# Optimization experiments

Hardware: AMD Instinct MI355X
Metric: run time of the kernel (lower is better)

## Reference

```python
import jax, jax.numpy as jnp
import numpy as np

D_MODEL = 1024
N_HEADS = 16
D_K = D_MODEL // N_HEADS
B, S = 2, 2048


def setup_inputs() -> dict:
    key = jax.random.key(0)
    ks = jax.random.split(key, 5)
    x = jax.random.normal(ks[0], (B, S, D_MODEL), dtype=jnp.float32)
    # causal 0/1 mask, broadcastable over batch and heads
    mask = jnp.tril(jnp.ones((S, S), dtype=jnp.int32))[None, None, :, :]
    scale = 1.0 / np.sqrt(D_MODEL)
    w_qkv_w = jax.random.normal(ks[1], (3 * D_MODEL, D_MODEL), dtype=jnp.float32) * scale
    w_qkv_b = jnp.zeros((3 * D_MODEL,), dtype=jnp.float32)
    w_o_w = jax.random.normal(ks[2], (D_MODEL, D_MODEL), dtype=jnp.float32) * scale
    w_o_b = jnp.zeros((D_MODEL,), dtype=jnp.float32)
    return {"x": x, "mask": mask, "w_qkv_w": w_qkv_w, "w_qkv_b": w_qkv_b,
            "w_o_w": w_o_w, "w_o_b": w_o_b}


def reference(x, mask, w_qkv_w, w_qkv_b, w_o_w, w_o_b):
    b, s, d = x.shape
    qkv = x @ w_qkv_w.T + w_qkv_b                       # [b, s, 3d]
    q, k, v = jnp.split(qkv, 3, axis=-1)
    # [b, h, s, dk]
    q = q.reshape(b, s, N_HEADS, D_K).transpose(0, 2, 1, 3)
    k = k.reshape(b, s, N_HEADS, D_K).transpose(0, 2, 1, 3)
    v = v.reshape(b, s, N_HEADS, D_K).transpose(0, 2, 1, 3)
    scores = jnp.einsum('bhqd,bhkd->bhqk', q, k) / jnp.sqrt(jnp.float32(D_K))
    scores = jnp.where(mask == 0, jnp.float32(-1e9), scores)
    attn = jax.nn.softmax(scores, axis=-1)
    out = jnp.einsum('bhqk,bhkd->bhqd', attn, v)        # [b, h, s, dk]
    out = out.transpose(0, 2, 1, 3).reshape(b, s, d)
    return out @ w_o_w.T + w_o_b
```

## Files before the change

kernel.cpp:

```cpp
#include <hip/hip_runtime.h>
#include <cstdint>
#include <cstddef>


typedef __attribute__((ext_vector_type(8))) short bf16x8;
typedef __attribute__((ext_vector_type(4))) float f32x4;
typedef __attribute__((ext_vector_type(4))) unsigned int u32x4;
typedef __attribute__((ext_vector_type(4))) unsigned short u16x4;
typedef __attribute__((ext_vector_type(8))) unsigned short u16x8;

__device__ __forceinline__ unsigned short f2b(float f) {
  unsigned int u = __float_as_uint(f);
  u = u + 0x7FFFu + ((u >> 16) & 1u);
  return (unsigned short)(u >> 16);
}
__device__ __forceinline__ unsigned short f2b_trunc(float f) {
  return (unsigned short)(__float_as_uint(f) >> 16);
}

__device__ __forceinline__ void gl_lds16(const unsigned short* g, unsigned short* s) {
  __builtin_amdgcn_global_load_lds((const __attribute__((address_space(1))) void*)g,
                                   (__attribute__((address_space(3))) void*)s, 16, 0, 0);
}

__global__ __launch_bounds__(256) void cvt_all(const float* __restrict__ x,
                                               const float* __restrict__ wq,
                                               const float* __restrict__ wo,
                                               unsigned short* __restrict__ xb,
                                               unsigned short* __restrict__ wqb,
                                               unsigned short* __restrict__ wob) {
  const int bid = blockIdx.x;
  const float* in;
  unsigned short* out;
  int base;
  if (bid < 4096)      { in = x;  out = xb;  base = bid; }
  else if (bid < 7168) { in = wq; out = wqb; base = bid - 4096; }
  else                 { in = wo; out = wob; base = bid - 7168; }
  const int idx = (base * 256 + threadIdx.x) * 4;
  f32x4 v = *(const f32x4*)(in + idx);
  u16x4 r;
  r[0] = f2b(v[0]); r[1] = f2b(v[1]); r[2] = f2b(v[2]); r[3] = f2b(v[3]);
  *(u16x4*)(out + idx) = r;
}

__global__ __launch_bounds__(256) void gemm_bt(const unsigned short* __restrict__ A,
                                               const unsigned short* __restrict__ W,
                                               const float* __restrict__ bias,
                                               unsigned short* __restrict__ Cb,
                                               unsigned short* __restrict__ vtb,
                                               int M, int N, int K, int qcols) {
  __shared__ unsigned short As[2][128 * 32];
  __shared__ unsigned short Bs[2][128 * 32];
  const int tid  = threadIdx.x;
  const int lane = tid & 63;
  const int w    = tid >> 6;
  const int wy   = w >> 1, wx = w & 1;
  const int l15  = lane & 15, quad = lane >> 4;
  const int xr2  = (l15 >> 1) & 3;
  const int m0 = blockIdx.y * 128, n0 = blockIdx.x * 128;

  const unsigned short* gA[2];
  const unsigned short* gB[2];
  int off[2];
#pragma unroll
  for (int p = 0; p < 2; ++p) {
    const int c = tid + p * 256;
    const int r = c >> 2;
    const int srcc = (c & 3) ^ ((r >> 1) & 3);
    gA[p] = A + (size_t)(m0 + r) * K + srcc * 8;
    gB[p] = W + (size_t)(n0 + r) * K + srcc * 8;
    off[p] = c * 8;
  }

  f32x4 acc[4][4];
#pragma unroll
  for (int i = 0; i < 4; ++i)
#pragma unroll
    for (int j = 0; j < 4; ++j) acc[i][j] = (f32x4){0.f, 0.f, 0.f, 0.f};

#pragma unroll
  for (int p = 0; p < 2; ++p) {
    gl_lds16(gA[p], &As[0][off[p]]);
    gl_lds16(gB[p], &Bs[0][off[p]]);
  }

  const int NIT = K >> 5;
  for (int it = 0; it < NIT; ++it) {
    __syncthreads();
    const int cur = it & 1;
    if (it + 1 < NIT) {
      const int kt = (it + 1) << 5;
#pragma unroll
      for (int p = 0; p < 2; ++p) {
        gl_lds16(gA[p] + kt, &As[cur ^ 1][off[p]]);
        gl_lds16(gB[p] + kt, &Bs[cur ^ 1][off[p]]);
      }
    }
    const unsigned short* Ac = As[cur];
    const unsigned short* Bc = Bs[cur];
    bf16x8 af[4], bfr[4];
#pragma unroll
    for (int i = 0; i < 4; ++i)
      af[i] = *(const bf16x8*)&Ac[(wy * 64 + i * 16 + l15) * 32 + (quad ^ xr2) * 8];
#pragma unroll
    for (int j = 0; j < 4; ++j)
      bfr[j] = *(const bf16x8*)&Bc[(wx * 64 + j * 16 + l15) * 32 + (quad ^ xr2) * 8];
#pragma unroll
    for (int i = 0; i < 4; ++i)
#pragma unroll
      for (int j = 0; j < 4; ++j)
        acc[i][j] = __builtin_amdgcn_mfma_f32_16x16x32_bf16(af[i], bfr[j], acc[i][j], 0, 0, 0);
  }

  const bool vblock = (n0 >= 2048);
#pragma unroll
  for (int i = 0; i < 4; ++i) {
    const int row = m0 + wy * 64 + i * 16 + quad * 4;
#pragma unroll
    for (int j = 0; j < 4; ++j) {
      const int col = n0 + wx * 64 + j * 16 + l15;
      const float bv = bias[col];
      if (!vblock) {
        const float sc = (col < qcols) ? 0.125f : 1.0f;
#pragma unroll
        for (int r = 0; r < 4; ++r)
          Cb[(size_t)(row + r) * N + col] = f2b((acc[i][j][r] + bv) * sc);
      } else {
        const int hd = col - 2048;
        const int bb = row >> 11, s = row & 2047;
        u16x4 ov;
#pragma unroll
        for (int r = 0; r < 4; ++r) ov[r] = f2b(acc[i][j][r] + bv);
        *(u16x4*)(vtb + ((size_t)(bb * 1024 + hd)) * 2048 + s) = ov;
      }
    }
  }
}

__global__ __launch_bounds__(256) void gemm_bt64(const unsigned short* __restrict__ A,
                                                 const unsigned short* __restrict__ W,
                                                 const float* __restrict__ bias,
                                                 float* __restrict__ Cf,
                                                 int M, int N, int K) {
  __shared__ unsigned short As[2][128 * 64];
  __shared__ unsigned short Bs[2][64 * 64];
  const int tid  = threadIdx.x;
  const int lane = tid & 63;
  const int w    = tid >> 6;
  const int wy   = w >> 1, wx = w & 1;
  const int l15  = lane & 15, quad = lane >> 4;
  const int xr   = l15 & 7;
  const int m0 = blockIdx.y * 128, n0 = blockIdx.x * 64;

  const unsigned short* gA[4];
  int offA[4];
#pragma unroll
  for (int p = 0; p < 4; ++p) {
    const int c = tid + p * 256;
    const int r = c >> 3;
    const int sc = ((c & 7) ^ (r & 7)) * 8;
    gA[p] = A + (size_t)(m0 + r) * K + sc;
    offA[p] = c * 8;
  }
  const unsigned short* gB[2];
  int offB[2];
#pragma unroll
  for (int p = 0; p < 2; ++p) {
    const int c = tid + p * 256;
    const int r = c >> 3;
    const int sc = ((c & 7) ^ (r & 7)) * 8;
    gB[p] = W + (size_t)(n0 + r) * K + sc;
    offB[p] = c * 8;
  }

  f32x4 acc[4][2];
#pragma unroll
  for (int i = 0; i < 4; ++i)
#pragma unroll
    for (int j = 0; j < 2; ++j) acc[i][j] = (f32x4){0.f, 0.f, 0.f, 0.f};

#pragma unroll
  for (int p = 0; p < 4; ++p) gl_lds16(gA[p], &As[0][offA[p]]);
#pragma unroll
  for (int p = 0; p < 2; ++p) gl_lds16(gB[p], &Bs[0][offB[p]]);

  const int NIT = K >> 6;
  for (int it = 0; it < NIT; ++it) {
    __syncthreads();
    const int cur = it & 1;
    if (it + 1 < NIT) {
      const int kt = (it + 1) << 6;
#pragma unroll
      for (int p = 0; p < 4; ++p) gl_lds16(gA[p] + kt, &As[cur ^ 1][offA[p]]);
#pragma unroll
      for (int p = 0; p < 2; ++p) gl_lds16(gB[p] + kt, &Bs[cur ^ 1][offB[p]]);
    }
    const unsigned short* Ac = As[cur];
    const unsigned short* Bc = Bs[cur];
#pragma unroll
    for (int kc = 0; kc < 2; ++kc) {
      bf16x8 af[4], bfr[2];
#pragma unroll
      for (int i = 0; i < 4; ++i)
        af[i] = *(const bf16x8*)&Ac[(wy * 64 + i * 16 + l15) * 64 + ((kc * 4 + quad) ^ xr) * 8];
#pragma unroll
      for (int j = 0; j < 2; ++j)
        bfr[j] = *(const bf16x8*)&Bc[(wx * 32 + j * 16 + l15) * 64 + ((kc * 4 + quad) ^ xr) * 8];
#pragma unroll
      for (int i = 0; i < 4; ++i)
#pragma unroll
        for (int j = 0; j < 2; ++j)
          acc[i][j] = __builtin_amdgcn_mfma_f32_16x16x32_bf16(af[i], bfr[j], acc[i][j], 0, 0, 0);
    }
  }

#pragma unroll
  for (int i = 0; i < 4; ++i) {
    const int row = m0 + wy * 64 + i * 16 + quad * 4;
#pragma unroll
    for (int j = 0; j < 2; ++j) {
      const int col = n0 + wx * 32 + j * 16 + l15;
      const float bv = bias[col];
#pragma unroll
      for (int r = 0; r < 4; ++r)
        Cf[(size_t)(row + r) * N + col] = acc[i][j][r] + bv;
    }
  }
}

__global__ __launch_bounds__(256, 3) void attn_fwd(const unsigned short* __restrict__ qkv,
                                                   const unsigned short* __restrict__ vt,
                                                   unsigned short* __restrict__ o) {
  __shared__ unsigned short Ks[2][64 * 64];
  __shared__ unsigned short Vs[2][64 * 64];
  __shared__ unsigned short pbuf[4][2][16 * 40];
  const int tid  = threadIdx.x;
  const int lane = tid & 63;
  const int w    = tid >> 6;
  const int wq   = w & 1;
  const int wk   = w >> 1;
  const int l15  = lane & 15, quad = lane >> 4;
  const int xr   = l15 & 7;
  const int bh = blockIdx.x, b = bh >> 4, h = bh & 15;
  const int y  = (int)blockIdx.y;
  const int qt = (y < 16) ? y : 47 - y;
  const int q0 = qt * 64;
  const int T = qt + 1;
  const int qs0 = q0 + wq * 32;
  const int qs1 = qs0 + 16;

  const unsigned short* gKd[2];
  const unsigned short* gVd[2];
  int doff[2];
#pragma unroll
  for (int p = 0; p < 2; ++p) {
    const int c = tid + p * 256;
    const int r = c >> 3;
    const int sc = ((c & 7) ^ (r & 7)) * 8;
    gKd[p] = qkv + (size_t)(b * 2048 + r) * 3072 + 1024 + h * 64 + sc;
    gVd[p] = vt + (size_t)(bh * 64 + r) * 2048 + sc;
    doff[p] = c * 8;
  }

  const unsigned short* qr0 = qkv + (size_t)(b * 2048 + qs0 + l15) * 3072 + h * 64;
  const unsigned short* qr1 = qkv + (size_t)(b * 2048 + qs1 + l15) * 3072 + h * 64;
  const bf16x8 bq[2][2] = {
    { *(const bf16x8*)(qr0 + quad * 8), *(const bf16x8*)(qr0 + 32 + quad * 8) },
    { *(const bf16x8*)(qr1 + quad * 8), *(const bf16x8*)(qr1 + 32 + quad * 8) } };

  bf16x8 vones;
#pragma unroll
  for (int k = 0; k < 8; ++k) vones[k] = (short)0x3F80;

  f32x4 acc[2][4];
#pragma unroll
  for (int i = 0; i < 2; ++i)
#pragma unroll
    for (int j = 0; j < 4; ++j) acc[i][j] = (f32x4){0.f, 0.f, 0.f, 0.f};
  f32x4 accL[2] = {(f32x4){0.f, 0.f, 0.f, 0.f}, (f32x4){0.f, 0.f, 0.f, 0.f}};

  unsigned short* P0 = pbuf[w][0];
  unsigned short* P1 = pbuf[w][1];

#pragma unroll
  for (int p = 0; p < 2; ++p) {
    gl_lds16(gKd[p], &Ks[0][doff[p]]);
    gl_lds16(gVd[p], &Vs[0][doff[p]]);
  }

  for (int t = 0; t < T; ++t) {
    __syncthreads();
    const int cur = t & 1;
    if (t + 1 < T) {
      const size_t ko = (size_t)(t + 1) * 64 * 3072;
      const int vo = (t + 1) * 64;
#pragma unroll
      for (int p = 0; p < 2; ++p) {
        gl_lds16(gKd[p] + ko, &Ks[cur ^ 1][doff[p]]);
        gl_lds16(gVd[p] + vo, &Vs[cur ^ 1][doff[p]]);
      }
    }
    const unsigned short* Kc = Ks[cur];
    const unsigned short* Vc = Vs[cur];
    const int kv0 = t * 64 + wk * 32;

    bf16x8 kA[2][2];
#pragma unroll
    for (int n = 0; n < 2; ++n) {
      const int row = wk * 32 + n * 16 + l15;
      kA[n][0] = *(const bf16x8*)&Kc[row * 64 + ((quad) ^ xr) * 8];
      kA[n][1] = *(const bf16x8*)&Kc[row * 64 + ((4 + quad) ^ xr) * 8];
    }
    f32x4 st[2][2];
#pragma unroll
    for (int s = 0; s < 2; ++s)
#pragma unroll
      for (int n = 0; n < 2; ++n) {
        f32x4 z = (f32x4){0.f, 0.f, 0.f, 0.f};
        z = __builtin_amdgcn_mfma_f32_16x16x32_bf16(kA[n][0], bq[s][0], z, 0, 0, 0);
        z = __builtin_amdgcn_mfma_f32_16x16x32_bf16(kA[n][1], bq[s][1], z, 0, 0, 0);
        st[s][n] = z;
      }
    bf16x8 av[4];
#pragma unroll
    for (int j = 0; j < 4; ++j) {
      const int row = j * 16 + l15;
      av[j] = *(const bf16x8*)&Vc[row * 64 + ((wk * 4 + quad) ^ xr) * 8];
    }
#pragma unroll
    for (int s = 0; s < 2; ++s) {
      unsigned short* P = s ? P1 : P0;
      const int qbase = s ? qs1 : qs0;
      if (kv0 + 31 > qbase) {
        const int qrow = qbase + l15;
#pragma unroll
        for (int n = 0; n < 2; ++n)
#pragma unroll
          for (int r = 0; r < 4; ++r)
            if (kv0 + n * 16 + quad * 4 + r > qrow) st[s][n][r] = -1e30f;
      }
#pragma unroll
      for (int n = 0; n < 2; ++n) {
#pragma unroll
        for (int r = 0; r < 4; ++r) st[s][n][r] = __expf(st[s][n][r]);
        u16x4 pw;
        pw[0] = f2b_trunc(st[s][n][0]); pw[1] = f2b_trunc(st[s][n][1]);
        pw[2] = f2b_trunc(st[s][n][2]); pw[3] = f2b_trunc(st[s][n][3]);
        *(u16x4*)&P[l15 * 40 + n * 16 + quad * 4] = pw;
      }
    }
#pragma unroll
    for (int s = 0; s < 2; ++s) {
      const unsigned short* P = s ? P1 : P0;
      const bf16x8 bp = *(const bf16x8*)&P[l15 * 40 + quad * 8];
      accL[s] = __builtin_amdgcn_mfma_f32_16x16x32_bf16(vones, bp, accL[s], 0, 0, 0);
#pragma unroll
      for (int j = 0; j < 4; ++j)
        acc[s][j] = __builtin_amdgcn_mfma_f32_16x16x32_bf16(av[j], bp, acc[s][j], 0, 0, 0);
    }
  }

  __syncthreads();
  float* cmbA = (float*)&Ks[0][0];
  float* cmbL = (float*)&Vs[0][0];
  if (wk == 1) {
#pragma unroll
    for (int s = 0; s < 2; ++s) {
      cmbL[(wq * 2 + s) * 64 + lane] = accL[s][0];
#pragma unroll
      for (int j = 0; j < 4; ++j)
        *(f32x4*)&cmbA[(((wq * 2 + s) * 4 + j) << 8) + lane * 4] = acc[s][j];
    }
  }
  __syncthreads();
  if (wk == 0) {
#pragma unroll
    for (int s = 0; s < 2; ++s) {
      const float lsum = accL[s][0] + cmbL[(wq * 2 + s) * 64 + lane];
      const float inv = 1.0f / lsum;
      const int qrow = (s ? qs1 : qs0) + l15;
      unsigned short* orow = o + (size_t)(b * 2048 + qrow) * 1024 + h * 64;
#pragma unroll
      for (int j = 0; j < 4; ++j) {
        const f32x4 oth = *(const f32x4*)&cmbA[(((wq * 2 + s) * 4 + j) << 8) + lane * 4];
        u16x4 ov;
        ov[0] = f2b((acc[s][j][0] + oth[0]) * inv);
        ov[1] = f2b((acc[s][j][1] + oth[1]) * inv);
        ov[2] = f2b((acc[s][j][2] + oth[2]) * inv);
        ov[3] = f2b((acc[s][j][3] + oth[3]) * inv);
        *(u16x4*)(orow + j * 16 + quad * 4) = ov;
      }
    }
  }
}

extern "C" void kernel_launch(void* const* d_in, const int* in_sizes, int n_in,
                              void* d_out, int out_size, void* d_ws, size_t ws_size,
                              hipStream_t stream) {
  const float* x       = (const float*)d_in[0];
  const float* w_qkv_w = (const float*)d_in[2];
  const float* w_qkv_b = (const float*)d_in[3];
  const float* w_o_w   = (const float*)d_in[4];
  const float* w_o_b   = (const float*)d_in[5];
  float* out = (float*)d_out;

  unsigned short* ws    = (unsigned short*)d_ws;
  unsigned short* xb    = ws;
  unsigned short* wqb   = xb   + (size_t)4096 * 1024;
  unsigned short* wob   = wqb  + (size_t)3072 * 1024;
  unsigned short* qkvb  = wob  + (size_t)1024 * 1024;
  unsigned short* vtb   = qkvb + (size_t)4096 * 3072;
  unsigned short* attnb = vtb  + (size_t)2048 * 2048;

  cvt_all<<<8192, 256, 0, stream>>>(x, w_qkv_w, w_o_w, xb, wqb, wob);
  gemm_bt<<<dim3(24, 32), 256, 0, stream>>>(xb, wqb, w_qkv_b, qkvb, vtb, 4096, 3072, 1024, 1024);
  attn_fwd<<<dim3(32, 32), 256, 0, stream>>>(qkvb, vtb, attnb);
  gemm_bt64<<<dim3(16, 32), 256, 0, stream>>>(attnb, wob, w_o_b, out, 4096, 1024, 1024);
}
```

Measured before the change: 179.1 us.

## Replace QKV GEMM with 256x256 tile, 8-wave pipelined kernel

Rewrites the QKV projection GEMM to use 256x256 block tiles with 512 threads, a K-step of 64, and a hand-scheduled double buffer. Global-to-LDS loads are split into quarters and interleaved between MFMA groups, with explicit vmcnt waits, raw barriers and s_setprio. This aims to raise arithmetic intensity and overlap memory with compute. The cost is far fewer blocks (192) than CUs and large LDS use per block, which may leave compute units idle.

```diff
diff --git a/kernel.cpp b/kernel.cpp
--- a/kernel.cpp
+++ b/kernel.cpp
@@ -21,6 +21,12 @@
 __device__ __forceinline__ void gl_lds16(const unsigned short* g, unsigned short* s) {
   __builtin_amdgcn_global_load_lds((const __attribute__((address_space(1))) void*)g,
                                    (__attribute__((address_space(3))) void*)s, 16, 0, 0);
+}
+
+__device__ __forceinline__ void barrier_mem() {
+  asm volatile("" ::: "memory");
+  __builtin_amdgcn_s_barrier();
+  asm volatile("" ::: "memory");
 }
 
 __global__ __launch_bounds__(256) void cvt_all(const float* __restrict__ x,
@@ -43,94 +49,145 @@
   *(u16x4*)(out + idx) = r;
 }
 
-__global__ __launch_bounds__(256) void gemm_bt(const unsigned short* __restrict__ A,
-                                               const unsigned short* __restrict__ W,
-                                               const float* __restrict__ bias,
-                                               unsigned short* __restrict__ Cb,
-                                               unsigned short* __restrict__ vtb,
-                                               int M, int N, int K, int qcols) {
-  __shared__ unsigned short As[2][128 * 32];
-  __shared__ unsigned short Bs[2][128 * 32];
+__global__ __launch_bounds__(512, 2) void gemm8(const unsigned short* __restrict__ A,
+                                                const unsigned short* __restrict__ W,
+                                                const float* __restrict__ bias,
+                                                unsigned short* __restrict__ Cb,
+                                                unsigned short* __restrict__ vtb,
+                                                int M, int N, int K, int qcols) {
+  __shared__ unsigned short As[2][256 * 64];
+  __shared__ unsigned short Bs[2][256 * 64];
   const int tid  = threadIdx.x;
   const int lane = tid & 63;
   const int w    = tid >> 6;
-  const int wy   = w >> 1, wx = w & 1;
+  const int wm   = w >> 2;
+  const int wn   = w & 3;
   const int l15  = lane & 15, quad = lane >> 4;
-  const int xr2  = (l15 >> 1) & 3;
-  const int m0 = blockIdx.y * 128, n0 = blockIdx.x * 128;
-
-  const unsigned short* gA[2];
-  const unsigned short* gB[2];
-  int off[2];
-#pragma unroll
-  for (int p = 0; p < 2; ++p) {
-    const int c = tid + p * 256;
-    const int r = c >> 2;
-    const int srcc = (c & 3) ^ ((r >> 1) & 3);
-    gA[p] = A + (size_t)(m0 + r) * K + srcc * 8;
-    gB[p] = W + (size_t)(n0 + r) * K + srcc * 8;
-    off[p] = c * 8;
-  }
-
-  f32x4 acc[4][4];
-#pragma unroll
-  for (int i = 0; i < 4; ++i)
+  const int xr   = l15 & 7;
+  const int m0 = blockIdx.y * 256, n0 = blockIdx.x * 256;
+
+  const int r    = tid >> 3;
+  const int slot = (tid & 7) ^ (r & 7);
+  const unsigned short* gAq = A + (size_t)(m0 + r) * K + slot * 8;
+  const unsigned short* gBq = W + (size_t)(n0 + r) * K + slot * 8;
+  const int coff = tid * 8;
+
+  f32x4 acc[8][4];
+#pragma unroll
+  for (int i = 0; i < 8; ++i)
 #pragma unroll
     for (int j = 0; j < 4; ++j) acc[i][j] = (f32x4){0.f, 0.f, 0.f, 0.f};
 
-#pragma unroll
-  for (int p = 0; p < 2; ++p) {
-    gl_lds16(gA[p], &As[0][off[p]]);
-    gl_lds16(gB[p], &Bs[0][off[p]]);
-  }
-
-  const int NIT = K >> 5;
-  for (int it = 0; it < NIT; ++it) {
-    __syncthreads();
-    const int cur = it & 1;
-    if (it + 1 < NIT) {
-      const int kt = (it + 1) << 5;
-#pragma unroll
-      for (int p = 0; p < 2; ++p) {
-        gl_lds16(gA[p] + kt, &As[cur ^ 1][off[p]]);
-        gl_lds16(gB[p] + kt, &Bs[cur ^ 1][off[p]]);
-      }
-    }
-    const unsigned short* Ac = As[cur];
-    const unsigned short* Bc = Bs[cur];
-    bf16x8 af[4], bfr[4];
-#pragma unroll
-    for (int i = 0; i < 4; ++i)
-      af[i] = *(const bf16x8*)&Ac[(wy * 64 + i * 16 + l15) * 32 + (quad ^ xr2) * 8];
+  const size_t q64K = (size_t)64 * K;
+#pragma unroll
+  for (int qb = 0; qb < 4; ++qb)
+    gl_lds16(gBq + (size_t)qb * q64K, &Bs[0][qb * 4096 + coff]);
+  gl_lds16(gAq + 0 * q64K, &As[0][0 * 4096 + coff]);
+  gl_lds16(gAq + 2 * q64K, &As[0][2 * 4096 + coff]);
+  gl_lds16(gAq + 1 * q64K, &As[0][1 * 4096 + coff]);
+  gl_lds16(gAq + 3 * q64K, &As[0][3 * 4096 + coff]);
+
+  const int rowA = (wm * 128 + l15) * 64;
+  const int colB = (wn * 64 + l15) * 64;
+  const int NKT = K >> 6;
+
+  bf16x8 af[4][2], bf[4][2];
+  for (int kt = 0; kt < NKT; ++kt) {
+    const int buf = kt & 1;
+    const unsigned short* Ab = As[buf];
+    const unsigned short* Bb = Bs[buf];
+    unsigned short* An = As[buf ^ 1];
+    unsigned short* Bn = Bs[buf ^ 1];
+    const size_t kof = (size_t)((kt + 1 < NKT) ? kt + 1 : NKT - 2) * 64;
+
+    gl_lds16(gBq + 0 * q64K + kof, &Bn[0 * 4096 + coff]);
+    gl_lds16(gBq + 1 * q64K + kof, &Bn[1 * 4096 + coff]);
+    asm volatile("s_waitcnt vmcnt(4)" ::: "memory");
+    barrier_mem();
+#pragma unroll
+    for (int i = 0; i < 4; ++i)
+#pragma unroll
+      for (int kc = 0; kc < 2; ++kc)
+        af[i][kc] = *(const bf16x8*)&Ab[rowA + i * 1024 + (((kc * 4 + quad) ^ xr) * 8)];
 #pragma unroll
     for (int j = 0; j < 4; ++j)
-      bfr[j] = *(const bf16x8*)&Bc[(wx * 64 + j * 16 + l15) * 32 + (quad ^ xr2) * 8];
-#pragma unroll
-    for (int i = 0; i < 4; ++i)
-#pragma unroll
-      for (int j = 0; j < 4; ++j)
-        acc[i][j] = __builtin_amdgcn_mfma_f32_16x16x32_bf16(af[i], bfr[j], acc[i][j], 0, 0, 0);
+#pragma unroll
+      for (int kc = 0; kc < 2; ++kc)
+        bf[j][kc] = *(const bf16x8*)&Bb[colB + j * 1024 + (((kc * 4 + quad) ^ xr) * 8)];
+    asm volatile("s_waitcnt lgkmcnt(0)" ::: "memory");
+    __builtin_amdgcn_sched_barrier(0);
+    __builtin_amdgcn_s_setprio(1);
+#pragma unroll
+    for (int i = 0; i < 4; ++i)
+#pragma unroll
+      for (int j = 0; j < 2; ++j)
+#pragma unroll
+        for (int kc = 0; kc < 2; ++kc)
+          acc[i][j] = __builtin_amdgcn_mfma_f32_16x16x32_bf16(af[i][kc], bf[j][kc], acc[i][j], 0, 0, 0);
+    __builtin_amdgcn_s_setprio(0);
+    gl_lds16(gBq + 2 * q64K + kof, &Bn[2 * 4096 + coff]);
+    gl_lds16(gBq + 3 * q64K + kof, &Bn[3 * 4096 + coff]);
+    __builtin_amdgcn_s_setprio(1);
+#pragma unroll
+    for (int i = 0; i < 4; ++i)
+#pragma unroll
+      for (int j = 2; j < 4; ++j)
+#pragma unroll
+        for (int kc = 0; kc < 2; ++kc)
+          acc[i][j] = __builtin_amdgcn_mfma_f32_16x16x32_bf16(af[i][kc], bf[j][kc], acc[i][j], 0, 0, 0);
+    __builtin_amdgcn_s_setprio(0);
+    gl_lds16(gAq + 0 * q64K + kof, &An[0 * 4096 + coff]);
+    gl_lds16(gAq + 2 * q64K + kof, &An[2 * 4096 + coff]);
+    asm volatile("s_waitcnt vmcnt(6)" ::: "memory");
+    barrier_mem();
+#pragma unroll
+    for (int i = 0; i < 4; ++i)
+#pragma unroll
+      for (int kc = 0; kc < 2; ++kc)
+        af[i][kc] = *(const bf16x8*)&Ab[rowA + 4096 + i * 1024 + (((kc * 4 + quad) ^ xr) * 8)];
+    asm volatile("s_waitcnt lgkmcnt(0)" ::: "memory");
+    __builtin_amdgcn_sched_barrier(0);
+    __builtin_amdgcn_s_setprio(1);
+#pragma unroll
+    for (int i = 0; i < 4; ++i)
+#pragma unroll
+      for (int j = 2; j < 4; ++j)
+#pragma unroll
+        for (int kc = 0; kc < 2; ++kc)
+          acc[4 + i][j] = __builtin_amdgcn_mfma_f32_16x16x32_bf16(af[i][kc], bf[j][kc], acc[4 + i][j], 0, 0, 0);
+    __builtin_amdgcn_s_setprio(0);
+    gl_lds16(gAq + 1 * q64K + kof, &An[1 * 4096 + coff]);
+    gl_lds16(gAq + 3 * q64K + kof, &An[3 * 4096 + coff]);
+    __builtin_amdgcn_s_setprio(1);
+#pragma unroll
+    for (int i = 0; i < 4; ++i)
+#pragma unroll
+      for (int j = 0; j < 2; ++j)
+#pragma unroll
+        for (int kc = 0; kc < 2; ++kc)
+          acc[4 + i][j] = __builtin_amdgcn_mfma_f32_16x16x32_bf16(af[i][kc], bf[j][kc], acc[4 + i][j], 0, 0, 0);
+    __builtin_amdgcn_s_setprio(0);
   }
 
   const bool vblock = (n0 >= 2048);
 #pragma unroll
-  for (int i = 0; i < 4; ++i) {
-    const int row = m0 + wy * 64 + i * 16 + quad * 4;
+  for (int i = 0; i < 8; ++i) {
+    const int row = m0 + wm * 128 + i * 16 + quad * 4;
 #pragma unroll
     for (int j = 0; j < 4; ++j) {
-      const int col = n0 + wx * 64 + j * 16 + l15;
+      const int col = n0 + wn * 64 + j * 16 + l15;
       const float bv = bias[col];
       if (!vblock) {
         const float sc = (col < qcols) ? 0.125f : 1.0f;
 #pragma unroll
-        for (int r = 0; r < 4; ++r)
-          Cb[(size_t)(row + r) * N + col] = f2b((acc[i][j][r] + bv) * sc);
+        for (int rr = 0; rr < 4; ++rr)
+          Cb[(size_t)(row + rr) * N + col] = f2b((acc[i][j][rr] + bv) * sc);
       } else {
         const int hd = col - 2048;
         const int bb = row >> 11, s = row & 2047;
         u16x4 ov;
 #pragma unroll
-        for (int r = 0; r < 4; ++r) ov[r] = f2b(acc[i][j][r] + bv);
+        for (int rr = 0; rr < 4; ++rr) ov[rr] = f2b(acc[i][j][rr] + bv);
         *(u16x4*)(vtb + ((size_t)(bb * 1024 + hd)) * 2048 + s) = ov;
       }
     }
@@ -413,7 +470,7 @@
   unsigned short* attnb = vtb  + (size_t)2048 * 2048;
 
   cvt_all<<<8192, 256, 0, stream>>>(x, w_qkv_w, w_o_w, xb, wqb, wob);
-  gemm_bt<<<dim3(24, 32), 256, 0, stream>>>(xb, wqb, w_qkv_b, qkvb, vtb, 4096, 3072, 1024, 1024);
+  gemm8<<<dim3(12, 16), 512, 0, stream>>>(xb, wqb, w_qkv_b, qkvb, vtb, 4096, 3072, 1024, 1024);
   attn_fwd<<<dim3(32, 32), 256, 0, stream>>>(qkvb, vtb, attnb);
   gemm_bt64<<<dim3(16, 32), 256, 0, stream>>>(attnb, wob, w_o_b, out, 4096, 1024, 1024);
 }
```

Result: no change. 180.1 us (+0.5%).

## Split attention work across 8 waves with one 16-row query strip each

Applied to the files above, without the earlier changes.

The attention kernel now runs 512 threads per block, with 8 waves, instead of 256. Each wave handles a single 16-row query strip rather than two, which halves per-wave register state for accumulators and Q fragments. The K/V tile loads are spread over more threads, so each thread issues one load instead of two. This raises wave-level parallelism and latency hiding per block. In exchange, more waves redundantly read the same K/V fragments from LDS, and the larger blocks synchronize at every barrier.

```diff
diff --git a/kernel.cpp b/kernel.cpp
--- a/kernel.cpp
+++ b/kernel.cpp
@@ -228,17 +228,17 @@
   }
 }
 
-__global__ __launch_bounds__(256, 3) void attn_fwd(const unsigned short* __restrict__ qkv,
+__global__ __launch_bounds__(512, 6) void attn_fwd(const unsigned short* __restrict__ qkv,
                                                    const unsigned short* __restrict__ vt,
                                                    unsigned short* __restrict__ o) {
   __shared__ unsigned short Ks[2][64 * 64];
   __shared__ unsigned short Vs[2][64 * 64];
-  __shared__ unsigned short pbuf[4][2][16 * 40];
+  __shared__ unsigned short pbuf[8][16 * 40];
   const int tid  = threadIdx.x;
   const int lane = tid & 63;
   const int w    = tid >> 6;
-  const int wq   = w & 1;
-  const int wk   = w >> 1;
+  const int wq   = w & 3;
+  const int wk   = w >> 2;
   const int l15  = lane & 15, quad = lane >> 4;
   const int xr   = l15 & 7;
   const int bh = blockIdx.x, b = bh >> 4, h = bh & 15;
@@ -246,47 +246,31 @@
   const int qt = (y < 16) ? y : 47 - y;
   const int q0 = qt * 64;
   const int T = qt + 1;
-  const int qs0 = q0 + wq * 32;
-  const int qs1 = qs0 + 16;
-
-  const unsigned short* gKd[2];
-  const unsigned short* gVd[2];
-  int doff[2];
-#pragma unroll
-  for (int p = 0; p < 2; ++p) {
-    const int c = tid + p * 256;
-    const int r = c >> 3;
-    const int sc = ((c & 7) ^ (r & 7)) * 8;
-    gKd[p] = qkv + (size_t)(b * 2048 + r) * 3072 + 1024 + h * 64 + sc;
-    gVd[p] = vt + (size_t)(bh * 64 + r) * 2048 + sc;
-    doff[p] = c * 8;
-  }
-
-  const unsigned short* qr0 = qkv + (size_t)(b * 2048 + qs0 + l15) * 3072 + h * 64;
-  const unsigned short* qr1 = qkv + (size_t)(b * 2048 + qs1 + l15) * 3072 + h * 64;
-  const bf16x8 bq[2][2] = {
-    { *(const bf16x8*)(qr0 + quad * 8), *(const bf16x8*)(qr0 + 32 + quad * 8) },
-    { *(const bf16x8*)(qr1 + quad * 8), *(const bf16x8*)(qr1 + 32 + quad * 8) } };
+  const int qs = q0 + wq * 16;
+
+  const int r  = tid >> 3;
+  const int sc = ((tid & 7) ^ (r & 7)) * 8;
+  const unsigned short* gKd = qkv + (size_t)(b * 2048 + r) * 3072 + 1024 + h * 64 + sc;
+  const unsigned short* gVd = vt + (size_t)(bh * 64 + r) * 2048 + sc;
+  const int doff = tid * 8;
+
+  const unsigned short* qr = qkv + (size_t)(b * 2048 + qs + l15) * 3072 + h * 64;
+  const bf16x8 bq[2] = { *(const bf16x8*)(qr + quad * 8),
+                         *(const bf16x8*)(qr + 32 + quad * 8) };
 
   bf16x8 vones;
 #pragma unroll
   for (int k = 0; k < 8; ++k) vones[k] = (short)0x3F80;
 
-  f32x4 acc[2][4];
-#pragma unroll
-  for (int i = 0; i < 2; ++i)
-#pragma unroll
-    for (int j = 0; j < 4; ++j) acc[i][j] = (f32x4){0.f, 0.f, 0.f, 0.f};
-  f32x4 accL[2] = {(f32x4){0.f, 0.f, 0.f, 0.f}, (f32x4){0.f, 0.f, 0.f, 0.f}};
-
-  unsigned short* P0 = pbuf[w][0];
-  unsigned short* P1 = pbuf[w][1];
-
-#pragma unroll
-  for (int p = 0; p < 2; ++p) {
-    gl_lds16(gKd[p], &Ks[0][doff[p]]);
-    gl_lds16(gVd[p], &Vs[0][doff[p]]);
-  }
+  f32x4 acc[4];
+#pragma unroll
+  for (int j = 0; j < 4; ++j) acc[j] = (f32x4){0.f, 0.f, 0.f, 0.f};
+  f32x4 accL = (f32x4){0.f, 0.f, 0.f, 0.f};
+
+  unsigned short* P = pbuf[w];
+
+  gl_lds16(gKd, &Ks[0][doff]);
+  gl_lds16(gVd, &Vs[0][doff]);
 
   for (int t = 0; t < T; ++t) {
     __syncthreads();
@@ -294,69 +278,53 @@
     if (t + 1 < T) {
       const size_t ko = (size_t)(t + 1) * 64 * 3072;
       const int vo = (t + 1) * 64;
-#pragma unroll
-      for (int p = 0; p < 2; ++p) {
-        gl_lds16(gKd[p] + ko, &Ks[cur ^ 1][doff[p]]);
-        gl_lds16(gVd[p] + vo, &Vs[cur ^ 1][doff[p]]);
-      }
+      gl_lds16(gKd + ko, &Ks[cur ^ 1][doff]);
+      gl_lds16(gVd + vo, &Vs[cur ^ 1][doff]);
     }
     const unsigned short* Kc = Ks[cur];
     const unsigned short* Vc = Vs[cur];
     const int kv0 = t * 64 + wk * 32;
 
-    bf16x8 kA[2][2];
+    f32x4 st[2];
 #pragma unroll
     for (int n = 0; n < 2; ++n) {
       const int row = wk * 32 + n * 16 + l15;
-      kA[n][0] = *(const bf16x8*)&Kc[row * 64 + ((quad) ^ xr) * 8];
-      kA[n][1] = *(const bf16x8*)&Kc[row * 64 + ((4 + quad) ^ xr) * 8];
-    }
-    f32x4 st[2][2];
-#pragma unroll
-    for (int s = 0; s < 2; ++s)
-#pragma unroll
-      for (int n = 0; n < 2; ++n) {
-        f32x4 z = (f32x4){0.f, 0.f, 0.f, 0.f};
-        z = __builtin_amdgcn_mfma_f32_16x16x32_bf16(kA[n][0], bq[s][0], z, 0, 0, 0);
-        z = __builtin_amdgcn_mfma_f32_16x16x32_bf16(kA[n][1], bq[s][1], z, 0, 0, 0);
-        st[s][n] = z;
-      }
+      const bf16x8 kA0 = *(const bf16x8*)&Kc[row * 64 + ((quad) ^ xr) * 8];
+      const bf16x8 kA1 = *(const bf16x8*)&Kc[row * 64 + ((4 + quad) ^ xr) * 8];
+      f32x4 z = (f32x4){0.f, 0.f, 0.f, 0.f};
+      z = __builtin_amdgcn_mfma_f32_16x16x32_bf16(kA0, bq[0], z, 0, 0, 0);
+      z = __builtin_amdgcn_mfma_f32_16x16x32_bf16(kA1, bq[1], z, 0, 0, 0);
+      st[n] = z;
+    }
     bf16x8 av[4];
 #pragma unroll
     for (int j = 0; j < 4; ++j) {
       const int row = j * 16 + l15;
       av[j] = *(const bf16x8*)&Vc[row * 64 + ((wk * 4 + quad) ^ xr) * 8];
     }
-#pragma unroll
-    for (int s = 0; s < 2; ++s) {
-      unsigned short* P = s ? P1 : P0;
-      const int qbase = s ? qs1 : qs0;
-      if (kv0 + 31 > qbase) {
-        const int qrow = qbase + l15;
-#pragma unroll
-        for (int n = 0; n < 2; ++n)
-#pragma unroll
-          for (int r = 0; r < 4; ++r)
-            if (kv0 + n * 16 + quad * 4 + r > qrow) st[s][n][r] = -1e30f;
-      }
-#pragma unroll
-      for (int n = 0; n < 2; ++n) {
-#pragma unroll
-        for (int r = 0; r < 4; ++r) st[s][n][r] = __expf(st[s][n][r]);
-        u16x4 pw;
-        pw[0] = f2b_trunc(st[s][n][0]); pw[1] = f2b_trunc(st[s][n][1]);
-        pw[2] = f2b_trunc(st[s][n][2]); pw[3] = f2b_trunc(st[s][n][3]);
-        *(u16x4*)&P[l15 * 40 + n * 16 + quad * 4] = pw;
-      }
-    }
-#pragma unroll
-    for (int s = 0; s < 2; ++s) {
-      const unsigned short* P = s ? P1 : P0;
+    if (kv0 + 31 > qs) {
+      const int qrow = qs + l15;
+#pragma unroll
+      for (int n = 0; n < 2; ++n)
+#pragma unroll
+        for (int rr = 0; rr < 4; ++rr)
+          if (kv0 + n * 16 + quad * 4 + rr > qrow) st[n][rr] = -1e30f;
+    }
+#pragma unroll
+    for (int n = 0; n < 2; ++n) {
+#pragma unroll
+      for (int rr = 0; rr < 4; ++rr) st[n][rr] = __expf(st[n][rr]);
+      u16x4 pw;
+      pw[0] = f2b_trunc(st[n][0]); pw[1] = f2b_trunc(st[n][1]);
+      pw[2] = f2b_trunc(st[n][2]); pw[3] = f2b_trunc(st[n][3]);
+      *(u16x4*)&P[l15 * 40 + n * 16 + quad * 4] = pw;
+    }
+    {
       const bf16x8 bp = *(const bf16x8*)&P[l15 * 40 + quad * 8];
-      accL[s] = __builtin_amdgcn_mfma_f32_16x16x32_bf16(vones, bp, accL[s], 0, 0, 0);
+      accL = __builtin_amdgcn_mfma_f32_16x16x32_bf16(vones, bp, accL, 0, 0, 0);
 #pragma unroll
       for (int j = 0; j < 4; ++j)
-        acc[s][j] = __builtin_amdgcn_mfma_f32_16x16x32_bf16(av[j], bp, acc[s][j], 0, 0, 0);
+        acc[j] = __builtin_amdgcn_mfma_f32_16x16x32_bf16(av[j], bp, acc[j], 0, 0, 0);
     }
   }
 
@@ -364,32 +332,26 @@
   float* cmbA = (float*)&Ks[0][0];
   float* cmbL = (float*)&Vs[0][0];
   if (wk == 1) {
-#pragma unroll
-    for (int s = 0; s < 2; ++s) {
-      cmbL[(wq * 2 + s) * 64 + lane] = accL[s][0];
-#pragma unroll
-      for (int j = 0; j < 4; ++j)
-        *(f32x4*)&cmbA[(((wq * 2 + s) * 4 + j) << 8) + lane * 4] = acc[s][j];
-    }
+    cmbL[wq * 64 + lane] = accL[0];
+#pragma unroll
+    for (int j = 0; j < 4; ++j)
+      *(f32x4*)&cmbA[((wq * 4 + j) << 8) + lane * 4] = acc[j];
   }
   __syncthreads();
   if (wk == 0) {
-#pragma unroll
-    for (int s = 0; s < 2; ++s) {
-      const float lsum = accL[s][0] + cmbL[(wq * 2 + s) * 64 + lane];
-      const float inv = 1.0f / lsum;
-      const int qrow = (s ? qs1 : qs0) + l15;
-      unsigned short* orow = o + (size_t)(b * 2048 + qrow) * 1024 + h * 64;
-#pragma unroll
-      for (int j = 0; j < 4; ++j) {
-        const f32x4 oth = *(const f32x4*)&cmbA[(((wq * 2 + s) * 4 + j) << 8) + lane * 4];
-        u16x4 ov;
-        ov[0] = f2b((acc[s][j][0] + oth[0]) * inv);
-        ov[1] = f2b((acc[s][j][1] + oth[1]) * inv);
-        ov[2] = f2b((acc[s][j][2] + oth[2]) * inv);
-        ov[3] = f2b((acc[s][j][3] + oth[3]) * inv);
-        *(u16x4*)(orow + j * 16 + quad * 4) = ov;
-      }
+    const float lsum = accL[0] + cmbL[wq * 64 + lane];
+    const float inv = 1.0f / lsum;
+    const int qrow = qs + l15;
+    unsigned short* orow = o + (size_t)(b * 2048 + qrow) * 1024 + h * 64;
+#pragma unroll
+    for (int j = 0; j < 4; ++j) {
+      const f32x4 oth = *(const f32x4*)&cmbA[((wq * 4 + j) << 8) + lane * 4];
+      u16x4 ov;
+      ov[0] = f2b((acc[j][0] + oth[0]) * inv);
+      ov[1] = f2b((acc[j][1] + oth[1]) * inv);
+      ov[2] = f2b((acc[j][2] + oth[2]) * inv);
+      ov[3] = f2b((acc[j][3] + oth[3]) * inv);
+      *(u16x4*)(orow + j * 16 + quad * 4) = ov;
     }
   }
 }
@@ -414,6 +376,6 @@
 
   cvt_all<<<8192, 256, 0, stream>>>(x, w_qkv_w, w_o_w, xb, wqb, wob);
   gemm_bt<<<dim3(24, 32), 256, 0, stream>>>(xb, wqb, w_qkv_b, qkvb, vtb, 4096, 3072, 1024, 1024);
-  attn_fwd<<<dim3(32, 32), 256, 0, stream>>>(qkvb, vtb, attnb);
+  attn_fwd<<<dim3(32, 32), 512, 0, stream>>>(qkvb, vtb, attnb);
   gemm_bt64<<<dim3(16, 32), 256, 0, stream>>>(attnb, wob, w_o_b, out, 4096, 1024, 1024);
 }
```

After: 179.2 us. About the same (+0.1%).

## Widen attention KV tile from 64 to 128 keys per iteration

Applied to the files above, without the earlier changes.

Each loop iteration now loads 128 keys and values instead of 64, so every wave handles 64 keys and the number of iterations and barriers is roughly halved. The P buffer is widened and XOR-swizzled to feed two MFMA k-steps, and the V layout is remapped to 128-wide rows. In exchange, shared memory roughly doubles and launch bounds drop from 3 to 2 blocks per CU, which lowers occupancy. On the diagonal, tiles now overshoot by up to 64 keys, so more masked work is wasted.

```diff
diff --git a/kernel.cpp b/kernel.cpp
--- a/kernel.cpp
+++ b/kernel.cpp
@@ -228,12 +228,12 @@
   }
 }
 
-__global__ __launch_bounds__(256, 3) void attn_fwd(const unsigned short* __restrict__ qkv,
+__global__ __launch_bounds__(256, 2) void attn_fwd(const unsigned short* __restrict__ qkv,
                                                    const unsigned short* __restrict__ vt,
                                                    unsigned short* __restrict__ o) {
-  __shared__ unsigned short Ks[2][64 * 64];
-  __shared__ unsigned short Vs[2][64 * 64];
-  __shared__ unsigned short pbuf[4][2][16 * 40];
+  __shared__ unsigned short Ks[2][128 * 64];
+  __shared__ unsigned short Vs[2][64 * 128];
+  __shared__ unsigned short pbuf[4][2][16 * 64];
   const int tid  = threadIdx.x;
   const int lane = tid & 63;
   const int w    = tid >> 6;
@@ -245,21 +245,29 @@
   const int y  = (int)blockIdx.y;
   const int qt = (y < 16) ? y : 47 - y;
   const int q0 = qt * 64;
-  const int T = qt + 1;
+  const int T = (qt >> 1) + 1;
   const int qs0 = q0 + wq * 32;
   const int qs1 = qs0 + 16;
 
-  const unsigned short* gKd[2];
-  const unsigned short* gVd[2];
-  int doff[2];
-#pragma unroll
-  for (int p = 0; p < 2; ++p) {
+  const unsigned short* gKd[4];
+  int dKoff[4];
+#pragma unroll
+  for (int p = 0; p < 4; ++p) {
     const int c = tid + p * 256;
     const int r = c >> 3;
     const int sc = ((c & 7) ^ (r & 7)) * 8;
     gKd[p] = qkv + (size_t)(b * 2048 + r) * 3072 + 1024 + h * 64 + sc;
-    gVd[p] = vt + (size_t)(bh * 64 + r) * 2048 + sc;
-    doff[p] = c * 8;
+    dKoff[p] = c * 8;
+  }
+  const unsigned short* gVd[4];
+  int dVoff[4];
+#pragma unroll
+  for (int p = 0; p < 4; ++p) {
+    const int c = tid + p * 256;
+    const int rv = c >> 4;
+    const int sv = ((c & 15) ^ (rv & 7)) * 8;
+    gVd[p] = vt + (size_t)(bh * 64 + rv) * 2048 + sv;
+    dVoff[p] = c * 8;
   }
 
   const unsigned short* qr0 = qkv + (size_t)(b * 2048 + qs0 + l15) * 3072 + h * 64;
@@ -283,80 +291,82 @@
   unsigned short* P1 = pbuf[w][1];
 
 #pragma unroll
-  for (int p = 0; p < 2; ++p) {
-    gl_lds16(gKd[p], &Ks[0][doff[p]]);
-    gl_lds16(gVd[p], &Vs[0][doff[p]]);
-  }
+  for (int p = 0; p < 4; ++p) gl_lds16(gKd[p], &Ks[0][dKoff[p]]);
+#pragma unroll
+  for (int p = 0; p < 4; ++p) gl_lds16(gVd[p], &Vs[0][dVoff[p]]);
 
   for (int t = 0; t < T; ++t) {
     __syncthreads();
     const int cur = t & 1;
     if (t + 1 < T) {
-      const size_t ko = (size_t)(t + 1) * 64 * 3072;
-      const int vo = (t + 1) * 64;
-#pragma unroll
-      for (int p = 0; p < 2; ++p) {
-        gl_lds16(gKd[p] + ko, &Ks[cur ^ 1][doff[p]]);
-        gl_lds16(gVd[p] + vo, &Vs[cur ^ 1][doff[p]]);
-      }
+      const size_t ko = (size_t)(t + 1) * 128 * 3072;
+      const int vo = (t + 1) * 128;
+#pragma unroll
+      for (int p = 0; p < 4; ++p) gl_lds16(gKd[p] + ko, &Ks[cur ^ 1][dKoff[p]]);
+#pragma unroll
+      for (int p = 0; p < 4; ++p) gl_lds16(gVd[p] + vo, &Vs[cur ^ 1][dVoff[p]]);
     }
     const unsigned short* Kc = Ks[cur];
     const unsigned short* Vc = Vs[cur];
-    const int kv0 = t * 64 + wk * 32;
-
-    bf16x8 kA[2][2];
-#pragma unroll
-    for (int n = 0; n < 2; ++n) {
-      const int row = wk * 32 + n * 16 + l15;
-      kA[n][0] = *(const bf16x8*)&Kc[row * 64 + ((quad) ^ xr) * 8];
-      kA[n][1] = *(const bf16x8*)&Kc[row * 64 + ((4 + quad) ^ xr) * 8];
-    }
-    f32x4 st[2][2];
-#pragma unroll
-    for (int s = 0; s < 2; ++s)
-#pragma unroll
-      for (int n = 0; n < 2; ++n) {
-        f32x4 z = (f32x4){0.f, 0.f, 0.f, 0.f};
-        z = __builtin_amdgcn_mfma_f32_16x16x32_bf16(kA[n][0], bq[s][0], z, 0, 0, 0);
-        z = __builtin_amdgcn_mfma_f32_16x16x32_bf16(kA[n][1], bq[s][1], z, 0, 0, 0);
-        st[s][n] = z;
-      }
-    bf16x8 av[4];
+    const int kv0 = t * 128 + wk * 64;
+
+    f32x4 st[2][4];
+#pragma unroll
+    for (int n = 0; n < 4; ++n) {
+      const int row = wk * 64 + n * 16 + l15;
+      const bf16x8 kA0 = *(const bf16x8*)&Kc[row * 64 + ((quad) ^ xr) * 8];
+      const bf16x8 kA1 = *(const bf16x8*)&Kc[row * 64 + ((4 + quad) ^ xr) * 8];
+      f32x4 z0 = (f32x4){0.f, 0.f, 0.f, 0.f};
+      z0 = __builtin_amdgcn_mfma_f32_16x16x32_bf16(kA0, bq[0][0], z0, 0, 0, 0);
+      z0 = __builtin_amdgcn_mfma_f32_16x16x32_bf16(kA1, bq[0][1], z0, 0, 0, 0);
+      st[0][n] = z0;
+      f32x4 z1 = (f32x4){0.f, 0.f, 0.f, 0.f};
+      z1 = __builtin_amdgcn_mfma_f32_16x16x32_bf16(kA0, bq[1][0], z1, 0, 0, 0);
+      z1 = __builtin_amdgcn_mfma_f32_16x16x32_bf16(kA1, bq[1][1], z1, 0, 0, 0);
+      st[1][n] = z1;
+    }
+    bf16x8 av[4][2];
 #pragma unroll
     for (int j = 0; j < 4; ++j) {
       const int row = j * 16 + l15;
-      av[j] = *(const bf16x8*)&Vc[row * 64 + ((wk * 4 + quad) ^ xr) * 8];
+      av[j][0] = *(const bf16x8*)&Vc[row * 128 + ((wk * 8 + quad) ^ xr) * 8];
+      av[j][1] = *(const bf16x8*)&Vc[row * 128 + ((wk * 8 + 4 + quad) ^ xr) * 8];
     }
 #pragma unroll
     for (int s = 0; s < 2; ++s) {
       unsigned short* P = s ? P1 : P0;
       const int qbase = s ? qs1 : qs0;
-      if (kv0 + 31 > qbase) {
+      if (kv0 + 63 > qbase) {
         const int qrow = qbase + l15;
 #pragma unroll
-        for (int n = 0; n < 2; ++n)
-#pragma unroll
-          for (int r = 0; r < 4; ++r)
-            if (kv0 + n * 16 + quad * 4 + r > qrow) st[s][n][r] = -1e30f;
-      }
-#pragma unroll
-      for (int n = 0; n < 2; ++n) {
-#pragma unroll
-        for (int r = 0; r < 4; ++r) st[s][n][r] = __expf(st[s][n][r]);
+        for (int n = 0; n < 4; ++n)
+#pragma unroll
+          for (int rr = 0; rr < 4; ++rr)
+            if (kv0 + n * 16 + quad * 4 + rr > qrow) st[s][n][rr] = -1e30f;
+      }
+#pragma unroll
+      for (int n = 0; n < 4; ++n) {
+#pragma unroll
+        for (int rr = 0; rr < 4; ++rr) st[s][n][rr] = __expf(st[s][n][rr]);
         u16x4 pw;
         pw[0] = f2b_trunc(st[s][n][0]); pw[1] = f2b_trunc(st[s][n][1]);
         pw[2] = f2b_trunc(st[s][n][2]); pw[3] = f2b_trunc(st[s][n][3]);
-        *(u16x4*)&P[l15 * 40 + n * 16 + quad * 4] = pw;
+        const int slot = n * 2 + (quad >> 1);
+        *(u16x4*)&P[l15 * 64 + ((slot ^ xr) * 8) + (quad & 1) * 4] = pw;
       }
     }
 #pragma unroll
     for (int s = 0; s < 2; ++s) {
       const unsigned short* P = s ? P1 : P0;
-      const bf16x8 bp = *(const bf16x8*)&P[l15 * 40 + quad * 8];
-      accL[s] = __builtin_amdgcn_mfma_f32_16x16x32_bf16(vones, bp, accL[s], 0, 0, 0);
-#pragma unroll
-      for (int j = 0; j < 4; ++j)
-        acc[s][j] = __builtin_amdgcn_mfma_f32_16x16x32_bf16(av[j], bp, acc[s][j], 0, 0, 0);
+      const bf16x8 bp0 = *(const bf16x8*)&P[l15 * 64 + ((quad ^ xr) * 8)];
+      const bf16x8 bp1 = *(const bf16x8*)&P[l15 * 64 + (((4 + quad) ^ xr) * 8)];
+      accL[s] = __builtin_amdgcn_mfma_f32_16x16x32_bf16(vones, bp0, accL[s], 0, 0, 0);
+      accL[s] = __builtin_amdgcn_mfma_f32_16x16x32_bf16(vones, bp1, accL[s], 0, 0, 0);
+#pragma unroll
+      for (int j = 0; j < 4; ++j) {
+        acc[s][j] = __builtin_amdgcn_mfma_f32_16x16x32_bf16(av[j][0], bp0, acc[s][j], 0, 0, 0);
+        acc[s][j] = __builtin_amdgcn_mfma_f32_16x16x32_bf16(av[j][1], bp1, acc[s][j], 0, 0, 0);
+      }
     }
   }
 
```

After: 180.3 us. About the same (+0.7%).
